# Kernel tuning notes

Measured on AMD Instinct MI355X. Metric: run time of the kernel, lower is better.

Reference implementation:

```python
import jax, jax.numpy as jnp
import numpy as np

IOU_THRESHOLD = 0.5

def cxcywh_to_xyxy(b):
    cx, cy, w, h = jnp.split(b, 4, axis=-1)
    return jnp.concatenate([cx - 0.5 * w, cy - 0.5 * h, cx + 0.5 * w, cy + 0.5 * h], axis=-1)

def batched_giou(p_xyxy, t_xyxy):
    # p_xyxy: [B, N, 4], t_xyxy: [B, T, 4] -> giou: [B, N, T]
    p = p_xyxy[:, :, None, :]  # [B, N, 1, 4]
    t = t_xyxy[:, None, :, :]  # [B, 1, T, 4]
    area_p = (p_xyxy[..., 2] - p_xyxy[..., 0]) * (p_xyxy[..., 3] - p_xyxy[..., 1])  # [B, N]
    area_t = (t_xyxy[..., 2] - t_xyxy[..., 0]) * (t_xyxy[..., 3] - t_xyxy[..., 1])  # [B, T]
    lt = jnp.maximum(p[..., :2], t[..., :2])
    rb = jnp.minimum(p[..., 2:], t[..., 2:])
    wh = jnp.clip(rb - lt, 0.0)
    inter = wh[..., 0] * wh[..., 1]  # [B, N, T]
    union = area_p[:, :, None] + area_t[:, None, :] - inter
    iou = inter / union
    # enclosing box
    lt_e = jnp.minimum(p[..., :2], t[..., :2])
    rb_e = jnp.maximum(p[..., 2:], t[..., 2:])
    wh_e = jnp.clip(rb_e - lt_e, 0.0)
    area_e = wh_e[..., 0] * wh_e[..., 1]
    return iou - (area_e - union) / area_e

def setup_inputs() -> dict:
    key = jax.random.key(0)
    k1, k2 = jax.random.split(key)
    B, N, T = 128, 900, 300
    pred_boxes = jax.random.uniform(k1, (B, N, 4), dtype=jnp.float32)
    target_boxes = jax.random.uniform(k2, (B, T, 4), dtype=jnp.float32)
    target_mask = jnp.ones((B, T), dtype=bool)
    return {"pred_boxes": pred_boxes, "target_boxes": target_boxes, "target_mask": target_mask}

def reference(pred_boxes, target_boxes, target_mask):
    # pred_boxes: [B, N, 4] cxcywh; target_boxes: [B, T, 4] cxcywh (padded)
    p_xyxy = cxcywh_to_xyxy(pred_boxes)
    t_xyxy = cxcywh_to_xyxy(target_boxes)
    giou = batched_giou(p_xyxy, t_xyxy)  # [B, N, T]
    max_iou = jnp.max(giou, axis=1)      # [B, T] best GIoU per target
    pred_idx = jnp.argmax(giou, axis=1)  # [B, T] matched query per target
    valid = target_mask & (max_iou >= IOU_THRESHOLD)  # [B, T] match kept
    return pred_idx, valid, max_iou
```

## Files before the change

kernel.cpp:

```cpp
#include <hip/hip_runtime.h>


#define BB 128
#define NN 900
#define TT 300
#define TCHUNK 64
#define TBLOCKS 5
#define NSPLIT 5
#define NPB 180
#define NPW 45

__global__ __launch_bounds__(256) void matcher_scan_kernel(
    const float* __restrict__ pred,
    const float* __restrict__ tgt,
    float2* __restrict__ part)
{
#pragma clang fp contract(off)
    __shared__ float4 sp[NPB];
    __shared__ float  sbest[256];
    __shared__ int    sbidx[256];

    const int ns  = blockIdx.x % NSPLIT;
    const int tc  = (blockIdx.x / NSPLIT) % TBLOCKS;
    const int b   = blockIdx.x / (NSPLIT * TBLOCKS);
    const int tid = threadIdx.x;
    const int tl  = tid & 63;
    const int ng  = tid >> 6;
    const int t   = tc * TCHUNK + tl;

    if (tid < NPB) {
        const float4 pb = ((const float4*)pred)[b * NN + ns * NPB + tid];
        float4 q;
        q.x = pb.x - 0.5f * pb.z;
        q.y = pb.y - 0.5f * pb.w;
        q.z = pb.x + 0.5f * pb.z;
        q.w = pb.y + 0.5f * pb.w;
        sp[tid] = q;
    }
    __syncthreads();

    float tx0 = 0.f, ty0 = 0.f, tx1 = 0.f, ty1 = 0.f, ta = 0.f;
    if (t < TT) {
        const float4 tb = ((const float4*)tgt)[b * TT + t];
        tx0 = tb.x - 0.5f * tb.z;
        ty0 = tb.y - 0.5f * tb.w;
        tx1 = tb.x + 0.5f * tb.z;
        ty1 = tb.y + 0.5f * tb.w;
        ta  = (tx1 - tx0) * (ty1 - ty0);
    }

    float best = -INFINITY;
    int   bidx = 0;
    const int k0 = ng * NPW;
    for (int k = 0; k < NPW; ++k) {
        const float4 p = sp[k0 + k];
        const float pa = (p.z - p.x) * (p.w - p.y);

        const float w   = fmaxf(fminf(p.z, tx1) - fmaxf(p.x, tx0), 0.f);
        const float h   = fmaxf(fminf(p.w, ty1) - fmaxf(p.y, ty0), 0.f);
        const float inter = w * h;
        const float uni   = pa + ta - inter;
        const float iou   = inter / uni;

        const float ew  = fmaxf(fmaxf(p.z, tx1) - fminf(p.x, tx0), 0.f);
        const float eh  = fmaxf(fmaxf(p.w, ty1) - fminf(p.y, ty0), 0.f);
        const float ea  = ew * eh;
        const float g   = iou - (ea - uni) / ea;

        if (g > best) { best = g; bidx = k0 + k; }
    }

    sbest[tid] = best;
    sbidx[tid] = bidx;
    __syncthreads();

    if (ng == 0 && t < TT) {
        for (int s = 1; s < 4; ++s) {
            const float v = sbest[s * 64 + tl];
            const int   i = sbidx[s * 64 + tl];
            if (v > best) { best = v; bidx = i; }
        }
        float2 pr;
        pr.x = best;
        pr.y = __int_as_float(ns * NPB + bidx);
        part[(b * TT + t) * NSPLIT + ns] = pr;
    }
}

__global__ __launch_bounds__(256) void matcher_reduce_kernel(
    const float2* __restrict__ part,
    const unsigned char* __restrict__ mask,
    float* __restrict__ out)
{
    const int bt = blockIdx.x * 256 + threadIdx.x;
    if (bt >= BB * TT) return;

    float best = -INFINITY;
    int   bidx = 0;
    for (int s = 0; s < NSPLIT; ++s) {
        const float2 pr = part[bt * NSPLIT + s];
        if (pr.x > best) { best = pr.x; bidx = __float_as_int(pr.y); }
    }
    const bool valid = (mask[bt] != 0) && (best >= 0.5f);
    out[bt]               = (float)bidx;
    out[BB * TT + bt]     = valid ? 1.f : 0.f;
    out[2 * BB * TT + bt] = best;
}

extern "C" void kernel_launch(void* const* d_in, const int* in_sizes, int n_in,
                              void* d_out, int out_size, void* d_ws, size_t ws_size,
                              hipStream_t stream) {
    const float* pred = (const float*)d_in[0];
    const float* tgt  = (const float*)d_in[1];
    const unsigned char* mask = (const unsigned char*)d_in[2];
    float* out = (float*)d_out;
    float2* part = (float2*)d_ws;

    matcher_scan_kernel<<<dim3(BB * TBLOCKS * NSPLIT), dim3(256), 0, stream>>>(
        pred, tgt, part);
    matcher_reduce_kernel<<<dim3((BB * TT + 255) / 256), dim3(256), 0, stream>>>(
        part, mask, out);
}
```

Measured before the change: 111.0 us.

## Use fast reciprocal division in scan with top-2 margin check and exact rescan

The main GIoU scan now divides with a hardware reciprocal plus one Newton correction instead of IEEE division, precomputes prediction areas in shared memory, and tracks both the best and second-best scores. A combine kernel recomputes the winning GIoU exactly. Targets whose top two candidates fall within a small margin are pushed to a flagged list, and a rescan kernel recomputes those exactly over all predictions. This aims to cut the cost of the divide-heavy inner loop while keeping argmax results exact, at the price of an extra memset, a third kernel launch, an atomic counter, and more workspace traffic.

Result: faster. 107.7 us (-3.0%).

```diff
diff --git a/kernel.cpp b/kernel.cpp
--- a/kernel.cpp
+++ b/kernel.cpp
@@ -9,16 +9,45 @@
 #define NSPLIT 5
 #define NPB 180
 #define NPW 45
+#define MARGIN 1e-5f
+
+__device__ __forceinline__ float fdiv_fast(float n, float d) {
+    float r = __builtin_amdgcn_rcpf(d);
+    float q = n * r;
+    float e = fmaf(-d, q, n);
+    return fmaf(e, r, q);
+}
+
+__device__ __forceinline__ float giou_exact(float4 pb, float4 tb) {
+#pragma clang fp contract(off)
+    float px0 = pb.x - 0.5f * pb.z, py0 = pb.y - 0.5f * pb.w;
+    float px1 = pb.x + 0.5f * pb.z, py1 = pb.y + 0.5f * pb.w;
+    float tx0 = tb.x - 0.5f * tb.z, ty0 = tb.y - 0.5f * tb.w;
+    float tx1 = tb.x + 0.5f * tb.z, ty1 = tb.y + 0.5f * tb.w;
+    float pa = (px1 - px0) * (py1 - py0);
+    float ta = (tx1 - tx0) * (ty1 - ty0);
+    float w  = fmaxf(fminf(px1, tx1) - fmaxf(px0, tx0), 0.f);
+    float h  = fmaxf(fminf(py1, ty1) - fmaxf(py0, ty0), 0.f);
+    float inter = w * h;
+    float uni   = pa + ta - inter;
+    float iou   = inter / uni;
+    float ew = fmaxf(fmaxf(px1, tx1) - fminf(px0, tx0), 0.f);
+    float eh = fmaxf(fmaxf(py1, ty1) - fminf(py0, ty0), 0.f);
+    float ea = ew * eh;
+    return iou - (ea - uni) / ea;
+}
 
 __global__ __launch_bounds__(256) void matcher_scan_kernel(
     const float* __restrict__ pred,
     const float* __restrict__ tgt,
-    float2* __restrict__ part)
+    float* __restrict__ pbest,
+    float* __restrict__ psec,
+    int*   __restrict__ pidx)
 {
-#pragma clang fp contract(off)
     __shared__ float4 sp[NPB];
-    __shared__ float  sbest[256];
-    __shared__ int    sbidx[256];
+    __shared__ float  spa[NPB];
+    __shared__ float  rbv[256], rsv[256];
+    __shared__ int    riv[256];
 
     const int ns  = blockIdx.x % NSPLIT;
     const int tc  = (blockIdx.x / NSPLIT) % TBLOCKS;
@@ -35,7 +64,8 @@
         q.y = pb.y - 0.5f * pb.w;
         q.z = pb.x + 0.5f * pb.z;
         q.w = pb.y + 0.5f * pb.w;
-        sp[tid] = q;
+        sp[tid]  = q;
+        spa[tid] = (q.z - q.x) * (q.w - q.y);
     }
     __syncthreads();
 
@@ -49,62 +79,124 @@
         ta  = (tx1 - tx0) * (ty1 - ty0);
     }
 
-    float best = -INFINITY;
+    float best = -INFINITY, second = -INFINITY;
     int   bidx = 0;
     const int k0 = ng * NPW;
+    #pragma unroll 5
     for (int k = 0; k < NPW; ++k) {
         const float4 p = sp[k0 + k];
-        const float pa = (p.z - p.x) * (p.w - p.y);
+        const float pa = spa[k0 + k];
 
         const float w   = fmaxf(fminf(p.z, tx1) - fmaxf(p.x, tx0), 0.f);
         const float h   = fmaxf(fminf(p.w, ty1) - fmaxf(p.y, ty0), 0.f);
         const float inter = w * h;
         const float uni   = pa + ta - inter;
-        const float iou   = inter / uni;
-
-        const float ew  = fmaxf(fmaxf(p.z, tx1) - fminf(p.x, tx0), 0.f);
-        const float eh  = fmaxf(fmaxf(p.w, ty1) - fminf(p.y, ty0), 0.f);
-        const float ea  = ew * eh;
-        const float g   = iou - (ea - uni) / ea;
-
-        if (g > best) { best = g; bidx = k0 + k; }
-    }
-
-    sbest[tid] = best;
-    sbidx[tid] = bidx;
+        const float iou   = fdiv_fast(inter, uni);
+
+        const float ew = fmaxf(fmaxf(p.z, tx1) - fminf(p.x, tx0), 0.f);
+        const float eh = fmaxf(fmaxf(p.w, ty1) - fminf(p.y, ty0), 0.f);
+        const float ea = ew * eh;
+        const float g  = iou - fdiv_fast(ea - uni, ea);
+
+        second = __builtin_amdgcn_fmed3f(g, best, second);
+        if (g > best) { bidx = k0 + k; }
+        best = fmaxf(best, g);
+    }
+
+    rbv[tid] = best; rsv[tid] = second; riv[tid] = bidx;
     __syncthreads();
 
     if (ng == 0 && t < TT) {
         for (int s = 1; s < 4; ++s) {
-            const float v = sbest[s * 64 + tl];
-            const int   i = sbidx[s * 64 + tl];
-            if (v > best) { best = v; bidx = i; }
-        }
-        float2 pr;
-        pr.x = best;
-        pr.y = __int_as_float(ns * NPB + bidx);
-        part[(b * TT + t) * NSPLIT + ns] = pr;
-    }
-}
-
-__global__ __launch_bounds__(256) void matcher_reduce_kernel(
-    const float2* __restrict__ part,
+            const float ob = rbv[s * 64 + tl];
+            const float os = rsv[s * 64 + tl];
+            const int   oi = riv[s * 64 + tl];
+            second = fmaxf(fminf(best, ob), fmaxf(second, os));
+            if (ob > best) { best = ob; bidx = oi; }
+        }
+        const int bt = b * TT + t;
+        pbest[ns * BB * TT + bt] = best;
+        psec [ns * BB * TT + bt] = second;
+        pidx [ns * BB * TT + bt] = ns * NPB + bidx;
+    }
+}
+
+__global__ __launch_bounds__(256) void matcher_combine_kernel(
+    const float* __restrict__ pbest,
+    const float* __restrict__ psec,
+    const int*   __restrict__ pidx,
+    const float* __restrict__ pred,
+    const float* __restrict__ tgt,
     const unsigned char* __restrict__ mask,
-    float* __restrict__ out)
+    float* __restrict__ out,
+    int*   __restrict__ counter,
+    int*   __restrict__ flagged)
 {
     const int bt = blockIdx.x * 256 + threadIdx.x;
     if (bt >= BB * TT) return;
 
-    float best = -INFINITY;
+    float best = -INFINITY, second = -INFINITY;
     int   bidx = 0;
     for (int s = 0; s < NSPLIT; ++s) {
-        const float2 pr = part[bt * NSPLIT + s];
-        if (pr.x > best) { best = pr.x; bidx = __float_as_int(pr.y); }
-    }
-    const bool valid = (mask[bt] != 0) && (best >= 0.5f);
-    out[bt]               = (float)bidx;
-    out[BB * TT + bt]     = valid ? 1.f : 0.f;
-    out[2 * BB * TT + bt] = best;
+        const float ob = pbest[s * BB * TT + bt];
+        const float os = psec [s * BB * TT + bt];
+        const int   oi = pidx [s * BB * TT + bt];
+        second = fmaxf(fminf(best, ob), fmaxf(second, os));
+        if (ob > best) { best = ob; bidx = oi; }
+    }
+
+    if (best - second > MARGIN) {
+        const int b = bt / TT;
+        const float4 pb = ((const float4*)pred)[b * NN + bidx];
+        const float4 tb = ((const float4*)tgt)[bt];
+        const float g = giou_exact(pb, tb);
+        const bool valid = (mask[bt] != 0) && (g >= 0.5f);
+        out[bt]               = (float)bidx;
+        out[BB * TT + bt]     = valid ? 1.f : 0.f;
+        out[2 * BB * TT + bt] = g;
+    } else {
+        const int pos = atomicAdd(counter, 1);
+        flagged[pos] = bt;
+    }
+}
+
+__global__ __launch_bounds__(256) void matcher_rescan_kernel(
+    const float* __restrict__ pred,
+    const float* __restrict__ tgt,
+    const unsigned char* __restrict__ mask,
+    const int*   __restrict__ counter,
+    const int*   __restrict__ flagged,
+    float* __restrict__ out)
+{
+    const int wave   = (blockIdx.x * 256 + threadIdx.x) >> 6;
+    const int lane   = threadIdx.x & 63;
+    const int nwaves = gridDim.x * 4;
+    const int cnt    = *counter;
+
+    for (int f = wave; f < cnt; f += nwaves) {
+        const int bt = flagged[f];
+        const int b  = bt / TT;
+        const float4 tb = ((const float4*)tgt)[bt];
+
+        float best = -INFINITY;
+        int   bidx = NN;
+        for (int n = lane; n < NN; n += 64) {
+            const float4 pb = ((const float4*)pred)[b * NN + n];
+            const float g = giou_exact(pb, tb);
+            if (g > best) { best = g; bidx = n; }
+        }
+        for (int off = 32; off >= 1; off >>= 1) {
+            const float ob = __shfl_xor(best, off);
+            const int   oi = __shfl_xor(bidx, off);
+            if (ob > best || (ob == best && oi < bidx)) { best = ob; bidx = oi; }
+        }
+        if (lane == 0) {
+            const bool valid = (mask[bt] != 0) && (best >= 0.5f);
+            out[bt]               = (float)bidx;
+            out[BB * TT + bt]     = valid ? 1.f : 0.f;
+            out[2 * BB * TT + bt] = best;
+        }
+    }
 }
 
 extern "C" void kernel_launch(void* const* d_in, const int* in_sizes, int n_in,
@@ -114,10 +206,19 @@
     const float* tgt  = (const float*)d_in[1];
     const unsigned char* mask = (const unsigned char*)d_in[2];
     float* out = (float*)d_out;
-    float2* part = (float2*)d_ws;
-
+
+    char* ws = (char*)d_ws;
+    int*   counter = (int*)ws;
+    int*   flagged = (int*)(ws + 64);
+    float* pbest   = (float*)(ws + 64 + BB * TT * 4);
+    float* psec    = (float*)(ws + 64 + BB * TT * 4 * 6);
+    int*   pidx    = (int*)  (ws + 64 + BB * TT * 4 * 11);
+
+    hipMemsetAsync(counter, 0, sizeof(int), stream);
     matcher_scan_kernel<<<dim3(BB * TBLOCKS * NSPLIT), dim3(256), 0, stream>>>(
-        pred, tgt, part);
-    matcher_reduce_kernel<<<dim3((BB * TT + 255) / 256), dim3(256), 0, stream>>>(
-        part, mask, out);
-}
+        pred, tgt, pbest, psec, pidx);
+    matcher_combine_kernel<<<dim3((BB * TT + 255) / 256), dim3(256), 0, stream>>>(
+        pbest, psec, pidx, pred, tgt, mask, out, counter, flagged);
+    matcher_rescan_kernel<<<dim3(64), dim3(256), 0, stream>>>(
+        pred, tgt, mask, counter, flagged, out);
+}
```
